# Optimization experiments

Measured on AMD Instinct MI355X. Metric: run time of the kernel, lower is better.

The kernel has to match this reference:

```python
import jax, jax.numpy as jnp
import numpy as np

B, S, D = 4, 2048, 1024
H, HD = 16, 64  # n_heads, head_dim (n_kv_heads == n_heads -> n_rep = 1)
WINDOW = 256
ROPE_THETA = 10000.0


def setup_inputs() -> dict:
    key = jax.random.key(0)
    ks = jax.random.split(key, 5)
    x = jax.random.normal(ks[0], (B, S, D), dtype=jnp.float32)
    scale = 0.02
    wq = jax.random.normal(ks[1], (D, D), dtype=jnp.float32) * scale
    wk = jax.random.normal(ks[2], (D, D), dtype=jnp.float32) * scale
    wv = jax.random.normal(ks[3], (D, D), dtype=jnp.float32) * scale
    wo = jax.random.normal(ks[4], (D, D), dtype=jnp.float32) * scale
    # RoPE frequencies: freqs_cis[t, i] = exp(1j * t / theta^(2i/HD)), i in [0, HD/2)
    inv_freq = 1.0 / (ROPE_THETA ** (jnp.arange(0, HD, 2, dtype=jnp.float32) / HD))
    t = jnp.arange(S, dtype=jnp.float32)
    ang = t[:, None] * inv_freq[None, :]  # [S, HD/2]
    return {"x": x, "freqs_cos": jnp.cos(ang), "freqs_sin": jnp.sin(ang),
            "wq": wq, "wk": wk, "wv": wv, "wo": wo}


def _apply_rope(xq, xk, cos, sin):
    # xq/xk: [B, S, H, HD]; cos/sin: [S, HD/2] broadcast as [1, S, 1, HD/2]
    def rot(v):
        vr = v.reshape(*v.shape[:-1], HD // 2, 2)
        v0, v1 = vr[..., 0], vr[..., 1]
        c = cos[None, :, None, :]
        s = sin[None, :, None, :]
        o0 = v0 * c - v1 * s
        o1 = v0 * s + v1 * c
        return jnp.stack([o0, o1], axis=-1).reshape(v.shape)
    return rot(xq), rot(xk)


def reference(x, freqs_cos, freqs_sin, wq, wk, wv, wo):
    b, s, _ = x.shape
    xq = (x @ wq.T).reshape(b, s, H, HD)
    xk = (x @ wk.T).reshape(b, s, H, HD)
    xv = (x @ wv.T).reshape(b, s, H, HD)
    xq, xk = _apply_rope(xq, xk, freqs_cos, freqs_sin)
    # [B, H, S, S] scores
    scores = jnp.einsum('bqhd,bkhd->bhqk', xq, xk) / jnp.sqrt(jnp.float32(HD))
    pos = jnp.arange(s)
    # masked (disallowed) when j > i (future) or i - j >= window
    bad = (pos[None, :] > pos[:, None]) | (pos[:, None] - pos[None, :] >= WINDOW)
    scores = jnp.where(bad[None, None], -jnp.inf, scores)
    attn = jax.nn.softmax(scores.astype(jnp.float32), axis=-1).astype(xq.dtype)
    out = jnp.einsum('bhqk,bkhd->bqhd', attn, xv).reshape(b, s, H * HD)
    return out @ wo.T
```

## Files before the change

### kernel.cpp

```cpp
#include <hip/hip_runtime.h>
#include <hip/hip_bf16.h>


typedef __bf16 bf16_t;
typedef __attribute__((ext_vector_type(8))) __bf16 bf16x8;
typedef __attribute__((ext_vector_type(4))) __bf16 bf16x4;
typedef __attribute__((ext_vector_type(4))) float f32x4;

#define MFMA16(a, b, c) __builtin_amdgcn_mfma_f32_16x16x32_bf16((a), (b), (c), 0, 0, 0)

__device__ __forceinline__ void async16(const void* g, void* l) {
    __builtin_amdgcn_global_load_lds(
        (const __attribute__((address_space(1))) unsigned int*)g,
        (__attribute__((address_space(3))) unsigned int*)l, 16, 0, 0);
}

#define BAR() do { asm volatile("" ::: "memory"); __builtin_amdgcn_s_barrier(); \
                   asm volatile("" ::: "memory"); } while (0)
#define VMC(N) asm volatile("s_waitcnt vmcnt(" #N ")" ::: "memory")

__global__ __launch_bounds__(256) void cvt_all(const float* __restrict__ x,
                                               const float* __restrict__ wq,
                                               const float* __restrict__ wk,
                                               const float* __restrict__ wv,
                                               const float* __restrict__ wo,
                                               bf16_t* __restrict__ xbf,
                                               bf16_t* __restrict__ wqkv,
                                               bf16_t* __restrict__ wobf) {
    const int blk = blockIdx.x;
    const float* s;
    bf16_t* d;
    int base;
    if (blk < 4096)      { s = x;  d = xbf;            base = blk; }
    else if (blk < 4608) { s = wq; d = wqkv;           base = blk - 4096; }
    else if (blk < 5120) { s = wk; d = wqkv + 1048576; base = blk - 4608; }
    else if (blk < 5632) { s = wv; d = wqkv + 2097152; base = blk - 5120; }
    else                 { s = wo; d = wobf;           base = blk - 5632; }
    const int i = (base * 256 + threadIdx.x) * 8;
    float4 a = *(const float4*)(s + i);
    float4 b = *(const float4*)(s + i + 4);
    bf16x8 o;
    o[0] = (bf16_t)a.x; o[1] = (bf16_t)a.y; o[2] = (bf16_t)a.z; o[3] = (bf16_t)a.w;
    o[4] = (bf16_t)b.x; o[5] = (bf16_t)b.y; o[6] = (bf16_t)b.z; o[7] = (bf16_t)b.w;
    *(bf16x8*)(d + i) = o;
}

__global__ __launch_bounds__(512, 1) __attribute__((amdgpu_waves_per_eu(2)))
void gemm192_qkv(const bf16_t* __restrict__ A, const bf16_t* __restrict__ Bw,
                 const float* __restrict__ fcos, const float* __restrict__ fsin,
                 bf16_t* __restrict__ Qo, bf16_t* __restrict__ Ko,
                 bf16_t* __restrict__ Vtmp, int M, int N, int K) {
    __shared__ __attribute__((aligned(16))) bf16_t As[32768];
    __shared__ __attribute__((aligned(16))) bf16_t Bs[24576];
    const int tid = threadIdx.x;
    const int l = tid & 63, w = tid >> 6;
    const int lr = l & 15, lg = l >> 4;
    const int wr = w >> 2, wc = w & 3;

    const int nwg = gridDim.x * gridDim.y;
    const int flat = blockIdx.y * gridDim.x + blockIdx.x;
    const int swz = (flat & 7) * (nwg >> 3) + (flat >> 3);
    const int bx = swz % gridDim.x, by = swz / gridDim.x;
    const long m0 = (long)by * 256, n0 = (long)bx * 192;
    const int NT = K >> 6;
    const int NI = NT >> 1;

    const int p  = w * 1024 + l * 16;
    const int pp = p ^ (((p >> 9) & 1) << 5);
    const int st = pp >> 10;
    const int rSt = (st >> 1) * 16 + ((pp >> 6) & 15);
    const int cSt = (st & 1) * 32 + ((pp >> 4) & 3) * 8;
    const bf16_t* aS = A  + (m0 + rSt) * K + cSt;
    const bf16_t* bS = Bw + (n0 + rSt) * K + cSt;
    const long uK = 64L * K;

    auto stageA = [&](int b, int u, int t) {
        async16(aS + (long)u * uK + (long)t * 64,
                (char*)As + b * 32768 + u * 8192 + w * 1024);
    };
    auto stageB = [&](int b, int u, int t) {
        async16(bS + (long)u * uK + (long)t * 64,
                (char*)Bs + b * 24576 + u * 8192 + w * 1024);
    };

    f32x4 acc[8][3] = {};
    bf16x8 afX[4], afY[4], bfX[3], bfY[3];
    const int swd = (lr & 8) << 2;

    auto loadAF = [&](int b, int mh, int ks, bf16x8 (&dst)[4]) {
#pragma unroll
        for (int mi = 0; mi < 4; ++mi) {
            const int off = (wr * 2 + mh) * 8192 + (mi * 2 + ks) * 1024 +
                            lr * 64 + lg * 16;
            dst[mi] = *(const bf16x8*)((const char*)As + b * 32768 + (off ^ swd));
        }
    };
    auto loadBF = [&](int b, int ks, bf16x8 (&dst)[3]) {
#pragma unroll
        for (int nj = 0; nj < 3; ++nj) {
            const int rg = wc * 48 + nj * 16 + lr;
            const int off = (rg >> 6) * 8192 + (((rg >> 4) & 3) * 2 + ks) * 1024 +
                            lr * 64 + lg * 16;
            dst[nj] = *(const bf16x8*)((const char*)Bs + b * 24576 + (off ^ swd));
        }
    };

#define QMM(MH, AF, BF) do {                                                   \
    __builtin_amdgcn_s_setprio(1);                                             \
    _Pragma("unroll")                                                          \
    for (int mi = 0; mi < 4; ++mi)                                             \
        _Pragma("unroll")                                                      \
        for (int nj = 0; nj < 3; ++nj)                                         \
            acc[(MH)*4+mi][nj] = MFMA16((AF)[mi], (BF)[nj], acc[(MH)*4+mi][nj]); \
    __builtin_amdgcn_s_setprio(0);                                             \
} while (0)

    stageA(0, 0, 0); stageA(0, 1, 0); stageA(0, 2, 0); stageA(0, 3, 0);
    stageB(0, 0, 0); stageB(0, 1, 0); stageB(0, 2, 0);
    stageB(1, 0, 1); stageB(1, 1, 1); stageB(1, 2, 1);
    VMC(3);
    BAR();

#pragma unroll 1
    for (int it = 0; it < NI - 1; ++it) {
        const int T = 2 * it;
        loadAF(0, 0, 0, afX); loadBF(0, 0, bfX);
        stageA(1, 0, T + 1); stageA(1, 1, T + 1);
        BAR(); QMM(0, afX, bfX); BAR();
        loadAF(0, 1, 0, afY);
        stageA(1, 2, T + 1); stageA(1, 3, T + 1);
        BAR(); QMM(1, afY, bfX); BAR();
        loadAF(0, 0, 1, afX); loadBF(0, 1, bfY);
        BAR(); QMM(0, afX, bfY); BAR();
        loadAF(0, 1, 1, afY);
        stageB(0, 0, T + 2);
        BAR(); QMM(1, afY, bfY); VMC(1); BAR();
        loadAF(1, 0, 0, afX); loadBF(1, 0, bfX);
        stageB(0, 1, T + 2); stageB(0, 2, T + 2);
        BAR(); QMM(0, afX, bfX); BAR();
        loadAF(1, 1, 0, afY);
        stageA(0, 0, T + 2); stageA(0, 1, T + 2);
        BAR(); QMM(1, afY, bfX); BAR();
        loadAF(1, 0, 1, afX); loadBF(1, 1, bfY);
        stageA(0, 2, T + 2); stageA(0, 3, T + 2);
        BAR(); QMM(0, afX, bfY); BAR();
        loadAF(1, 1, 1, afY);
        stageB(1, 0, T + 3); stageB(1, 1, T + 3); stageB(1, 2, T + 3);
        BAR(); QMM(1, afY, bfY); VMC(3); BAR();
    }

    {
        loadAF(0, 0, 0, afX); loadBF(0, 0, bfX);
        stageA(1, 0, NT - 1); stageA(1, 1, NT - 1);
        BAR(); QMM(0, afX, bfX); BAR();
        loadAF(0, 1, 0, afY);
        stageA(1, 2, NT - 1); stageA(1, 3, NT - 1);
        BAR(); QMM(1, afY, bfX); BAR();
        loadAF(0, 0, 1, afX); loadBF(0, 1, bfY);
        BAR(); QMM(0, afX, bfY); BAR();
        loadAF(0, 1, 1, afY);
        BAR(); QMM(1, afY, bfY);
        VMC(0); BAR();
        loadAF(1, 0, 0, afX); loadBF(1, 0, bfX);
        QMM(0, afX, bfX);
        loadAF(1, 1, 0, afY);
        QMM(1, afY, bfX);
        loadAF(1, 0, 1, afX); loadBF(1, 1, bfY);
        QMM(0, afX, bfY);
        loadAF(1, 1, 1, afY);
        QMM(1, afY, bfY);
    }
#undef QMM

#pragma unroll
    for (int nj = 0; nj < 3; ++nj) {
        const int cbase = (int)n0 + wc * 48 + nj * 16;
        const int cls = cbase >> 10;
        const int c = cbase + lr;
        if (cls == 2) {
            bf16_t* vp = Vtmp + (c - 2048);
#pragma unroll
            for (int ai = 0; ai < 8; ++ai)
#pragma unroll
                for (int j = 0; j < 4; ++j) {
                    const long t = m0 + wr * 128 + ai * 16 + lg * 4 + j;
                    vp[t * 1024] = (bf16_t)acc[ai][nj][j];
                }
        } else {
            const int d = c & 63;
            const int p2 = d >> 1;
            const int h = (c >> 6) & 15;
            const float sgn = (lr & 1) ? 1.f : -1.f;
            bf16_t* qk = (cls == 0) ? Qo : Ko;
#pragma unroll
            for (int ai = 0; ai < 8; ++ai)
#pragma unroll
                for (int j = 0; j < 4; ++j) {
                    const long t = m0 + wr * 128 + ai * 16 + lg * 4 + j;
                    const int s = (int)(t & 2047);
                    const int bb = (int)(t >> 11);
                    const float v = acc[ai][nj][j];
                    const float pv = __shfl_xor(v, 1);
                    const float cc = fcos[s * 32 + p2];
                    const float ss = fsin[s * 32 + p2];
                    const float o = v * cc + sgn * (pv * ss);
                    qk[((long)(bb * 16 + h) * 2048 + s) * 64 + d] = (bf16_t)o;
                }
        }
    }
}

__global__ __launch_bounds__(256) void vt_transpose(const bf16_t* __restrict__ V,
                                                    bf16_t* __restrict__ VT) {
    __shared__ __attribute__((aligned(16))) bf16_t vt[64][72];
    const int blk = blockIdx.x;
    const int st = blk & 31, bh = blk >> 5;
    const int h = bh & 15, b = bh >> 4;
    const int s0 = st << 6;
    const int tid = threadIdx.x;
    const int i = tid >> 2, dq = (tid & 3) << 4;
    const int s = s0 + i;

    const bf16_t* base = V + (long)(b * 2048 + s) * 1024 + h * 64 + dq;
    bf16x8 v0v = *(const bf16x8*)(base);
    bf16x8 v1v = *(const bf16x8*)(base + 8);

    *(bf16x8*)&vt[i][dq] = v0v;
    *(bf16x8*)&vt[i][dq + 8] = v1v;
    __syncthreads();
    const int d = tid >> 2, sb = (tid & 3) << 4;
    bf16x8 o0, o1;
#pragma unroll
    for (int j = 0; j < 8; ++j) {
        const int f = ((j & 3) << 1) | ((j >> 2) & 1);
        o0[j] = vt[sb + f][d];
        o1[j] = vt[sb + 8 + f][d];
    }
    const long va = ((long)bh * 64 + d) * 2048 + s0 + sb;
    *(bf16x8*)(VT + va) = o0;
    *(bf16x8*)(VT + va + 8) = o1;
}

template <typename OUT>
__global__ __launch_bounds__(512, 2) void gemm256(const bf16_t* __restrict__ A,
                                                  const bf16_t* __restrict__ Bw,
                                                  OUT* __restrict__ C,
                                                  int M, int N, int K) {
    __shared__ __attribute__((aligned(16))) bf16_t As[49152];
    __shared__ __attribute__((aligned(16))) bf16_t Bs[24576];
    const int tid = threadIdx.x;
    const int l = tid & 63, w = tid >> 6;
    const int lr = l & 15, lg = l >> 4;
    const int wr = w >> 1, wc = w & 1;

    const int nwg = gridDim.x * gridDim.y;
    const int flat = blockIdx.y * gridDim.x + blockIdx.x;
    const int swz = (flat & 7) * (nwg >> 3) + (flat >> 3);
    const int bx = swz % gridDim.x, by = swz / gridDim.x;
    const long m0 = (long)by * 256, n0 = (long)bx * 128;
    const int NT = K >> 6;

    int rS[2], cS[2];
#pragma unroll
    for (int i = 0; i < 2; ++i) {
        const int p  = i * 8192 + w * 1024 + l * 16;
        const int pp = p ^ (((p >> 9) & 1) << 5);
        const int st = pp >> 10;
        rS[i] = (st >> 1) * 16 + ((pp >> 6) & 15);
        cS[i] = (st & 1) * 32 + ((pp >> 4) & 3) * 8;
    }
    const bf16_t* aSrc0 = A  + (m0 + rS[0]) * K + cS[0];
    const bf16_t* aSrc1 = A  + (m0 + rS[1]) * K + cS[1];
    const bf16_t* bSrc0 = Bw + (n0 + rS[0]) * K + cS[0];
    const bf16_t* bSrc1 = Bw + (n0 + rS[1]) * K + cS[1];
    const long hK = 128L * K;

    auto stageA = [&](int b, int h, int t) {
        char* d = (char*)As + b * 32768 + h * 16384 + w * 1024;
        const long o = (long)h * hK + (long)t * 64;
        async16(aSrc0 + o, d);
        async16(aSrc1 + o, d + 8192);
    };
    auto stageB = [&](int b, int t) {
        char* d = (char*)Bs + b * 16384 + w * 1024;
        const long o = (long)t * 64;
        async16(bSrc0 + o, d);
        async16(bSrc1 + o, d + 8192);
    };

    f32x4 acc[4][4] = {};
    bf16x8 af[4][2], blo[2][2], bhi[2][2];
    const int swd = (lr & 8) << 2;

    auto loadA = [&](int b) {
#pragma unroll
        for (int mi = 0; mi < 4; ++mi)
#pragma unroll
            for (int ks = 0; ks < 2; ++ks) {
                const int ra = (wr & 1) * 64 + mi * 16 + lr;
                const int off = ((ra >> 4) * 2 + ks) * 1024 + (ra & 15) * 64 + lg * 16;
                af[mi][ks] = *(const bf16x8*)((const char*)As + b * 32768 +
                                              (wr >> 1) * 16384 + (off ^ swd));
            }
    };
    auto loadB = [&](int b, int nh, bf16x8 (&dst)[2][2]) {
#pragma unroll
        for (int nj = 0; nj < 2; ++nj)
#pragma unroll
            for (int ks = 0; ks < 2; ++ks) {
                const int rb = wc * 64 + (nh * 2 + nj) * 16 + lr;
                const int off = ((rb >> 4) * 2 + ks) * 1024 + (rb & 15) * 64 + lg * 16;
                dst[nj][ks] = *(const bf16x8*)((const char*)Bs + b * 16384 +
                                               (off ^ swd));
            }
    };

#define QMM(NH, BF) do {                                                       \
    __builtin_amdgcn_s_setprio(1);                                             \
    _Pragma("unroll")                                                          \
    for (int mi = 0; mi < 4; ++mi) {                                           \
        acc[mi][(NH)*2]   = MFMA16(af[mi][0], (BF)[0][0], acc[mi][(NH)*2]);    \
        acc[mi][(NH)*2]   = MFMA16(af[mi][1], (BF)[0][1], acc[mi][(NH)*2]);    \
        acc[mi][(NH)*2+1] = MFMA16(af[mi][0], (BF)[1][0], acc[mi][(NH)*2+1]);  \
        acc[mi][(NH)*2+1] = MFMA16(af[mi][1], (BF)[1][1], acc[mi][(NH)*2+1]);  \
    }                                                                          \
    __builtin_amdgcn_s_setprio(0);                                             \
} while (0)

    stageA(0, 0, 0); stageA(0, 1, 0); stageB(0, 0);
    stageA(1, 0, 1); stageA(1, 1, 1); stageB(1, 1);
    VMC(6);
    BAR();

    int bc = 0;
#pragma unroll 1
    for (int t = 0; t < NT - 2; ++t) {
        const int bn = (bc + 2 >= 3) ? bc - 1 : bc + 2;
        loadA(bc); loadB(bc, 0, blo); stageA(bn, 0, t + 2); stageA(bn, 1, t + 2);
        BAR(); QMM(0, blo); BAR();
        loadB(bc, 1, bhi); stageB(bn, t + 2);
        BAR(); QMM(1, bhi);
        if (t < NT - 3) { VMC(6); } else { VMC(0); }
        BAR();
        bc = (bc + 1 >= 3) ? 0 : bc + 1;
    }
    {
        loadA(bc); loadB(bc, 0, blo);
        QMM(0, blo);
        loadB(bc, 1, bhi);
        QMM(1, bhi);
        const int b2 = (bc + 1 >= 3) ? 0 : bc + 1;
        loadA(b2); loadB(b2, 0, blo);
        QMM(0, blo);
        loadB(b2, 1, bhi);
        QMM(1, bhi);
    }
#undef QMM

#pragma unroll
    for (int mi = 0; mi < 4; ++mi)
#pragma unroll
        for (int ni = 0; ni < 4; ++ni)
#pragma unroll
            for (int j = 0; j < 4; ++j) {
                long r = m0 + wr * 64 + mi * 16 + lg * 4 + j;
                long c = n0 + wc * 64 + ni * 16 + lr;
                C[r * N + c] = (OUT)acc[mi][ni][j];
            }
}

__global__ __launch_bounds__(256, 2) void attn_win4(const bf16_t* __restrict__ Q,
                                                    const bf16_t* __restrict__ Kb,
                                                    const bf16_t* __restrict__ VT,
                                                    bf16_t* __restrict__ Ao) {
    __shared__ __attribute__((aligned(16))) bf16_t kld[5 * 4096];
    __shared__ __attribute__((aligned(16))) bf16_t vld[5 * 4096];
    const int raw = blockIdx.x;
    const int mswz = ((raw & 7) << 8) | (raw >> 3);
    const int qt = mswz & 31, bh = mswz >> 5;
    const int h = bh & 15, b = bh >> 4;
    const int l = threadIdx.x & 63, w = threadIdx.x >> 6;
    const int lr = l & 15, lg = l >> 4;
    const int q0 = qt * 64 + w * 16;
    const int q = q0 + lr;
    const int tb = qt - 4;

    const bf16_t* Qp = Q + (long)bh * 2048 * 64;
    const bf16_t* Kp = Kb + (long)bh * 2048 * 64;
    const bf16_t* Vp = VT + (long)bh * 64 * 2048;

#pragma unroll
    for (int u = 0; u < 5; ++u) {
        const int kt = tb + u;
        const int kt64 = (kt < 0 ? 0 : kt) * 64;
#pragma unroll
        for (int part = 0; part < 2; ++part) {
            const int seg = w * 2 + part;
            const int r = seg * 8 + (l >> 3);
            const int sc = (l & 7) ^ ((r >> 1) & 7);
            async16(Kp + (long)(kt64 + r) * 64 + sc * 8,
                    (char*)kld + u * 8192 + seg * 1024);
            async16(Vp + (long)r * 2048 + kt64 + sc * 8,
                    (char*)vld + u * 8192 + seg * 1024);
        }
    }

    const bf16x8 qb0 = *(const bf16x8*)&Qp[q * 64 + lg * 8];
    const bf16x8 qb1 = *(const bf16x8*)&Qp[q * 64 + 32 + lg * 8];

    __syncthreads();

    float mrun = -1000.f, lsum = 0.f;
    f32x4 o0 = {0.f, 0.f, 0.f, 0.f}, o1 = {0.f, 0.f, 0.f, 0.f};
    f32x4 o2 = {0.f, 0.f, 0.f, 0.f}, o3 = {0.f, 0.f, 0.f, 0.f};
    const int swv = (lr >> 1) & 7;

    const char* kbase;
    const char* vbase;
    int k0s;

#define QKCORE(HH, MM)                                                           \
        const int row_ = (HH) * 32 + 2 * lr + (MM);                              \
        const int sw_ = (row_ >> 1) & 7;                                         \
        bf16x8 k0_ = *(const bf16x8*)(kbase + row_ * 128 + ((lg ^ sw_) << 4));   \
        bf16x8 k1_ = *(const bf16x8*)(kbase + row_ * 128 + (((4 + lg) ^ sw_) << 4)); \
        f32x4 s_ = {0.f, 0.f, 0.f, 0.f};                                         \
        s_ = MFMA16(k0_, qb0, s_);                                               \
        s_ = MFMA16(k1_, qb1, s_);

#define QKF_F(DST, HH, MM)                                                       \
    f32x4 DST; { QKCORE(HH, MM)                                                  \
        const int kb_ = k0s + (HH) * 32 + (MM) + lg * 8;                         \
        DST[0] = ((kb_ >= 0) & ((unsigned)(q - kb_) < 256u))         ? s_[0] * 0.125f : -1e30f; \
        DST[1] = ((kb_ + 2 >= 0) & ((unsigned)(q - kb_ - 2) < 256u)) ? s_[1] * 0.125f : -1e30f; \
        DST[2] = ((kb_ + 4 >= 0) & ((unsigned)(q - kb_ - 4) < 256u)) ? s_[2] * 0.125f : -1e30f; \
        DST[3] = ((kb_ + 6 >= 0) & ((unsigned)(q - kb_ - 6) < 256u)) ? s_[3] * 0.125f : -1e30f; \
    }

#define QKF_U(DST, HH, MM)                                                       \
    f32x4 DST; { QKCORE(HH, MM)                                                  \
        const int d_ = q - (k0s + (HH) * 32 + (MM) + lg * 8);                    \
        DST[0] = (d_ < 256)     ? s_[0] * 0.125f : -1e30f;                       \
        DST[1] = (d_ - 2 < 256) ? s_[1] * 0.125f : -1e30f;                       \
        DST[2] = (d_ - 4 < 256) ? s_[2] * 0.125f : -1e30f;                       \
        DST[3] = (d_ - 6 < 256) ? s_[3] * 0.125f : -1e30f;                       \
    }

#define QKF_L(DST, HH, MM)                                                       \
    f32x4 DST; { QKCORE(HH, MM)                                                  \
        const int d_ = q - (k0s + (HH) * 32 + (MM) + lg * 8);                    \
        DST[0] = (d_ >= 0)     ? s_[0] * 0.125f : -1e30f;                        \
        DST[1] = (d_ - 2 >= 0) ? s_[1] * 0.125f : -1e30f;                        \
        DST[2] = (d_ - 4 >= 0) ? s_[2] * 0.125f : -1e30f;                        \
        DST[3] = (d_ - 6 >= 0) ? s_[3] * 0.125f : -1e30f;                        \
    }

#define QKF_N(DST, HH, MM)                                                       \
    f32x4 DST; { QKCORE(HH, MM)                                                  \
        DST[0] = s_[0] * 0.125f; DST[1] = s_[1] * 0.125f;                        \
        DST[2] = s_[2] * 0.125f; DST[3] = s_[3] * 0.125f;                        \
    }

#define EXV(S_) {                                                                \
        S_[0] = __expf(S_[0] - mnew); S_[1] = __expf(S_[1] - mnew);              \
        S_[2] = __expf(S_[2] - mnew); S_[3] = __expf(S_[3] - mnew);              \
        rs += (S_[0] + S_[1]) + (S_[2] + S_[3]); }

#define PVF(NT, HH, PB) {                                                        \
        bf16x8 va_ = *(const bf16x8*)(vbase + ((NT) * 16 + lr) * 128 +           \
                                      ((((HH) * 4 + lg) ^ swv) << 4));           \
        o##NT = MFMA16(va_, PB, o##NT); }

#define TILEBODY(QKM) {                                                          \
        QKM(sA, 0, 0) QKM(sB, 0, 1) QKM(sC, 1, 0) QKM(sD, 1, 1)                  \
        float tm = fmaxf(fmaxf(fmaxf(sA[0], sA[1]), fmaxf(sA[2], sA[3])),        \
                         fmaxf(fmaxf(sB[0], sB[1]), fmaxf(sB[2], sB[3])));       \
        tm = fmaxf(tm, fmaxf(fmaxf(fmaxf(sC[0], sC[1]), fmaxf(sC[2], sC[3])),    \
                             fmaxf(fmaxf(sD[0], sD[1]), fmaxf(sD[2], sD[3]))));  \
        tm = fmaxf(tm, __shfl_xor(tm, 16));                                      \
        tm = fmaxf(tm, __shfl_xor(tm, 32));                                      \
        const float mnew = fmaxf(mrun, tm);                                      \
        const float alpha = __expf(mrun - mnew);                                 \
        mrun = mnew;                                                             \
        float rs = 0.f;                                                          \
        EXV(sA) EXV(sB) EXV(sC) EXV(sD)                                          \
        rs += __shfl_xor(rs, 16);                                                \
        rs += __shfl_xor(rs, 32);                                                \
        lsum = lsum * alpha + rs;                                                \
        o0[0] *= alpha; o0[1] *= alpha; o0[2] *= alpha; o0[3] *= alpha;          \
        o1[0] *= alpha; o1[1] *= alpha; o1[2] *= alpha; o1[3] *= alpha;          \
        o2[0] *= alpha; o2[1] *= alpha; o2[2] *= alpha; o2[3] *= alpha;          \
        o3[0] *= alpha; o3[1] *= alpha; o3[2] *= alpha; o3[3] *= alpha;          \
        bf16x8 pb0, pb1;                                                         \
        pb0[0] = (bf16_t)sA[0]; pb0[1] = (bf16_t)sA[1]; pb0[2] = (bf16_t)sA[2]; pb0[3] = (bf16_t)sA[3]; \
        pb0[4] = (bf16_t)sB[0]; pb0[5] = (bf16_t)sB[1]; pb0[6] = (bf16_t)sB[2]; pb0[7] = (bf16_t)sB[3]; \
        pb1[0] = (bf16_t)sC[0]; pb1[1] = (bf16_t)sC[1]; pb1[2] = (bf16_t)sC[2]; pb1[3] = (bf16_t)sC[3]; \
        pb1[4] = (bf16_t)sD[0]; pb1[5] = (bf16_t)sD[1]; pb1[6] = (bf16_t)sD[2]; pb1[7] = (bf16_t)sD[3]; \
        PVF(0, 0, pb0) PVF(1, 0, pb0) PVF(2, 0, pb0) PVF(3, 0, pb0)              \
        PVF(0, 1, pb1) PVF(1, 1, pb1) PVF(2, 1, pb1) PVF(3, 1, pb1)              \
    }

#define SETT(U) kbase = (const char*)kld + (U) * 8192;                           \
                vbase = (const char*)vld + (U) * 8192;                           \
                k0s = (tb + (U)) * 64;

    if (qt >= 4) {
        SETT(0) TILEBODY(QKF_U)
        SETT(1) TILEBODY(QKF_N)
        SETT(2) TILEBODY(QKF_N)
        SETT(3) TILEBODY(QKF_N)
        SETT(4) TILEBODY(QKF_L)
    } else {
#pragma unroll
        for (int u = 0; u < 5; ++u) {
            SETT(u) TILEBODY(QKF_F)
        }
    }
#undef SETT
#undef TILEBODY
#undef QKF_F
#undef QKF_U
#undef QKF_L
#undef QKF_N
#undef QKCORE
#undef EXV
#undef PVF

    const float rinv = 1.0f / lsum;
    bf16_t* aor = Ao + ((long)(b * 2048) + q) * 1024 + h * 64;
#define EPI(NT, OA_) {                                                           \
        bf16x4 ov_;                                                             \
        ov_[0] = (bf16_t)(OA_[0] * rinv); ov_[1] = (bf16_t)(OA_[1] * rinv);      \
        ov_[2] = (bf16_t)(OA_[2] * rinv); ov_[3] = (bf16_t)(OA_[3] * rinv);      \
        *(bf16x4*)(aor + (NT) * 16 + lg * 4) = ov_; }
    EPI(0, o0) EPI(1, o1) EPI(2, o2) EPI(3, o3)
#undef EPI
}

extern "C" void kernel_launch(void* const* d_in, const int* in_sizes, int n_in,
                              void* d_out, int out_size, void* d_ws, size_t ws_size,
                              hipStream_t stream) {
    (void)in_sizes; (void)n_in; (void)out_size; (void)ws_size;
    const float* x    = (const float*)d_in[0];
    const float* fcos = (const float*)d_in[1];
    const float* fsin = (const float*)d_in[2];
    const float* wq   = (const float*)d_in[3];
    const float* wk   = (const float*)d_in[4];
    const float* wv   = (const float*)d_in[5];
    const float* wo   = (const float*)d_in[6];
    float* out = (float*)d_out;

    char* ws = (char*)d_ws;
    bf16_t* xbf  = (bf16_t*)(ws);
    bf16_t* wqkv = (bf16_t*)(ws + 16777216);
    bf16_t* wobf = (bf16_t*)(ws + 23068672);
    bf16_t* vtmp = (bf16_t*)(ws + 25165824);
    bf16_t* qbuf = (bf16_t*)(ws + 41943040);
    bf16_t* kbuf = (bf16_t*)(ws + 75497472);
    bf16_t* vtb  = (bf16_t*)(ws + 92274688);
    bf16_t* aob  = xbf;

    cvt_all<<<6144, 256, 0, stream>>>(x, wq, wk, wv, wo, xbf, wqkv, wobf);

    gemm192_qkv<<<dim3(16, 32), 512, 0, stream>>>(xbf, wqkv, fcos, fsin,
                                                  qbuf, kbuf, vtmp,
                                                  8192, 3072, 1024);
    vt_transpose<<<2048, 256, 0, stream>>>(vtmp, vtb);
    attn_win4<<<2048, 256, 0, stream>>>(qbuf, kbuf, vtb, aob);
    gemm256<float><<<dim3(8, 32), 512, 0, stream>>>(aob, wobf, out, 8192, 1024, 1024);
}
```

Baseline: 130.1 us.

## Fuse V transpose into QKV GEMM epilogue and transpose RoPE tables

The QKV GEMM epilogue now stages V tiles through reused LDS scratch and writes them directly in the transposed per-head layout that attention expects. This removes the separate vt_transpose kernel and its extra round trip of V through global memory. RoPE cos/sin tables are also transposed once inside the conversion kernel, so the Q/K epilogue can load them as float4 along the sequence axis. The cost is a more complex epilogue that depends on LDS reuse after the main loop having no hazards.

After: 126.9 us. 2.5% less time.

```diff
diff --git a/kernel.cpp b/kernel.cpp
--- a/kernel.cpp
+++ b/kernel.cpp
@@ -18,16 +18,29 @@
 #define BAR() do { asm volatile("" ::: "memory"); __builtin_amdgcn_s_barrier(); \
                    asm volatile("" ::: "memory"); } while (0)
 #define VMC(N) asm volatile("s_waitcnt vmcnt(" #N ")" ::: "memory")
+#define LGKM0() asm volatile("s_waitcnt lgkmcnt(0)" ::: "memory")
 
 __global__ __launch_bounds__(256) void cvt_all(const float* __restrict__ x,
                                                const float* __restrict__ wq,
                                                const float* __restrict__ wk,
                                                const float* __restrict__ wv,
                                                const float* __restrict__ wo,
+                                               const float* __restrict__ fcos,
+                                               const float* __restrict__ fsin,
                                                bf16_t* __restrict__ xbf,
                                                bf16_t* __restrict__ wqkv,
-                                               bf16_t* __restrict__ wobf) {
+                                               bf16_t* __restrict__ wobf,
+                                               float* __restrict__ fcosT,
+                                               float* __restrict__ fsinT) {
     const int blk = blockIdx.x;
+    if (blk >= 6144) {
+        const int p = blk - 6144;
+        for (int s = threadIdx.x; s < 2048; s += 256) {
+            fcosT[p * 2048 + s] = fcos[s * 32 + p];
+            fsinT[p * 2048 + s] = fsin[s * 32 + p];
+        }
+        return;
+    }
     const float* s;
     bf16_t* d;
     int base;
@@ -47,9 +60,9 @@
 
 __global__ __launch_bounds__(512, 1) __attribute__((amdgpu_waves_per_eu(2)))
 void gemm192_qkv(const bf16_t* __restrict__ A, const bf16_t* __restrict__ Bw,
-                 const float* __restrict__ fcos, const float* __restrict__ fsin,
+                 const float* __restrict__ fcosT, const float* __restrict__ fsinT,
                  bf16_t* __restrict__ Qo, bf16_t* __restrict__ Ko,
-                 bf16_t* __restrict__ Vtmp, int M, int N, int K) {
+                 bf16_t* __restrict__ VT, int M, int N, int K) {
     __shared__ __attribute__((aligned(16))) bf16_t As[32768];
     __shared__ __attribute__((aligned(16))) bf16_t Bs[24576];
     const int tid = threadIdx.x;
@@ -172,73 +185,71 @@
     }
 #undef QMM
 
+    bf16_t* scr = (w < 6) ? (bf16_t*)((char*)As + w * 4608)
+                          : (bf16_t*)((char*)Bs + (w - 6) * 4608);
+    asm volatile("" ::: "memory");
+
 #pragma unroll
     for (int nj = 0; nj < 3; ++nj) {
         const int cbase = (int)n0 + wc * 48 + nj * 16;
         const int cls = cbase >> 10;
-        const int c = cbase + lr;
         if (cls == 2) {
-            bf16_t* vp = Vtmp + (c - 2048);
 #pragma unroll
             for (int ai = 0; ai < 8; ++ai)
 #pragma unroll
-                for (int j = 0; j < 4; ++j) {
-                    const long t = m0 + wr * 128 + ai * 16 + lg * 4 + j;
-                    vp[t * 1024] = (bf16_t)acc[ai][nj][j];
+                for (int j = 0; j < 4; ++j)
+                    scr[(ai * 16 + lg * 4 + j) * 18 + lr] = (bf16_t)acc[ai][nj][j];
+            LGKM0();
+            asm volatile("" ::: "memory");
+            const int ch = l & 15;
+            const int g0 = l >> 4;
+            const int d16 = cbase - 2048 + ch;
+            const int hh = d16 >> 6, dd = d16 & 63;
+            const long T0 = m0 + wr * 128;
+            const int bb = (int)(T0 >> 11);
+            const int s0 = (int)(T0 & 2047);
+            bf16_t* vrow = VT + ((long)((bb * 16 + hh) * 64 + dd) * 2048) + s0;
+#pragma unroll
+            for (int qq = 0; qq < 4; ++qq) {
+                const int grp = g0 + qq * 4;
+                bf16x8 o;
+#pragma unroll
+                for (int j = 0; j < 8; ++j) {
+                    const int f = ((j & 3) << 1) | (j >> 2);
+                    o[j] = scr[(grp * 8 + f) * 18 + ch];
                 }
+                *(bf16x8*)(vrow + grp * 8) = o;
+            }
+            LGKM0();
+            asm volatile("" ::: "memory");
         } else {
-            const int d = c & 63;
-            const int p2 = d >> 1;
-            const int h = (c >> 6) & 15;
+            const int c = cbase + lr;
+            const int dd = c & 63;
+            const int p2 = dd >> 1;
+            const int hh = (c >> 6) & 15;
             const float sgn = (lr & 1) ? 1.f : -1.f;
             bf16_t* qk = (cls == 0) ? Qo : Ko;
-#pragma unroll
-            for (int ai = 0; ai < 8; ++ai)
-#pragma unroll
-                for (int j = 0; j < 4; ++j) {
-                    const long t = m0 + wr * 128 + ai * 16 + lg * 4 + j;
-                    const int s = (int)(t & 2047);
-                    const int bb = (int)(t >> 11);
-                    const float v = acc[ai][nj][j];
-                    const float pv = __shfl_xor(v, 1);
-                    const float cc = fcos[s * 32 + p2];
-                    const float ss = fsin[s * 32 + p2];
-                    const float o = v * cc + sgn * (pv * ss);
-                    qk[((long)(bb * 16 + h) * 2048 + s) * 64 + d] = (bf16_t)o;
-                }
+            const float* cT = fcosT + p2 * 2048;
+            const float* sT = fsinT + p2 * 2048;
+#pragma unroll
+            for (int ai = 0; ai < 8; ++ai) {
+                const long t0 = m0 + wr * 128 + ai * 16 + lg * 4;
+                const int s0 = (int)(t0 & 2047);
+                const int bb = (int)(t0 >> 11);
+                const float4 cc = *(const float4*)(cT + s0);
+                const float4 ss = *(const float4*)(sT + s0);
+                bf16_t* row = qk + ((long)(bb * 16 + hh) * 2048 + s0) * 64 + dd;
+                const float v0 = acc[ai][nj][0], pv0 = __shfl_xor(acc[ai][nj][0], 1);
+                const float v1 = acc[ai][nj][1], pv1 = __shfl_xor(acc[ai][nj][1], 1);
+                const float v2 = acc[ai][nj][2], pv2 = __shfl_xor(acc[ai][nj][2], 1);
+                const float v3 = acc[ai][nj][3], pv3 = __shfl_xor(acc[ai][nj][3], 1);
+                row[0]       = (bf16_t)(v0 * cc.x + sgn * (pv0 * ss.x));
+                row[64]      = (bf16_t)(v1 * cc.y + sgn * (pv1 * ss.y));
+                row[128]     = (bf16_t)(v2 * cc.z + sgn * (pv2 * ss.z));
+                row[192]     = (bf16_t)(v3 * cc.w + sgn * (pv3 * ss.w));
+            }
         }
     }
-}
-
-__global__ __launch_bounds__(256) void vt_transpose(const bf16_t* __restrict__ V,
-                                                    bf16_t* __restrict__ VT) {
-    __shared__ __attribute__((aligned(16))) bf16_t vt[64][72];
-    const int blk = blockIdx.x;
-    const int st = blk & 31, bh = blk >> 5;
-    const int h = bh & 15, b = bh >> 4;
-    const int s0 = st << 6;
-    const int tid = threadIdx.x;
-    const int i = tid >> 2, dq = (tid & 3) << 4;
-    const int s = s0 + i;
-
-    const bf16_t* base = V + (long)(b * 2048 + s) * 1024 + h * 64 + dq;
-    bf16x8 v0v = *(const bf16x8*)(base);
-    bf16x8 v1v = *(const bf16x8*)(base + 8);
-
-    *(bf16x8*)&vt[i][dq] = v0v;
-    *(bf16x8*)&vt[i][dq + 8] = v1v;
-    __syncthreads();
-    const int d = tid >> 2, sb = (tid & 3) << 4;
-    bf16x8 o0, o1;
-#pragma unroll
-    for (int j = 0; j < 8; ++j) {
-        const int f = ((j & 3) << 1) | ((j >> 2) & 1);
-        o0[j] = vt[sb + f][d];
-        o1[j] = vt[sb + 8 + f][d];
-    }
-    const long va = ((long)bh * 64 + d) * 2048 + s0 + sb;
-    *(bf16x8*)(VT + va) = o0;
-    *(bf16x8*)(VT + va + 8) = o1;
 }
 
 template <typename OUT>
@@ -551,21 +562,22 @@
     float* out = (float*)d_out;
 
     char* ws = (char*)d_ws;
-    bf16_t* xbf  = (bf16_t*)(ws);
-    bf16_t* wqkv = (bf16_t*)(ws + 16777216);
-    bf16_t* wobf = (bf16_t*)(ws + 23068672);
-    bf16_t* vtmp = (bf16_t*)(ws + 25165824);
-    bf16_t* qbuf = (bf16_t*)(ws + 41943040);
-    bf16_t* kbuf = (bf16_t*)(ws + 75497472);
-    bf16_t* vtb  = (bf16_t*)(ws + 92274688);
-    bf16_t* aob  = xbf;
-
-    cvt_all<<<6144, 256, 0, stream>>>(x, wq, wk, wv, wo, xbf, wqkv, wobf);
-
-    gemm192_qkv<<<dim3(16, 32), 512, 0, stream>>>(xbf, wqkv, fcos, fsin,
-                                                  qbuf, kbuf, vtmp,
+    bf16_t* xbf   = (bf16_t*)(ws);
+    bf16_t* wqkv  = (bf16_t*)(ws + 16777216);
+    bf16_t* wobf  = (bf16_t*)(ws + 23068672);
+    float*  fcosT = (float*)(ws + 25165824);
+    float*  fsinT = (float*)(ws + 25427968);
+    bf16_t* qbuf  = (bf16_t*)(ws + 41943040);
+    bf16_t* kbuf  = (bf16_t*)(ws + 75497472);
+    bf16_t* vtb   = (bf16_t*)(ws + 92274688);
+    bf16_t* aob   = xbf;
+
+    cvt_all<<<6176, 256, 0, stream>>>(x, wq, wk, wv, wo, fcos, fsin,
+                                      xbf, wqkv, wobf, fcosT, fsinT);
+
+    gemm192_qkv<<<dim3(16, 32), 512, 0, stream>>>(xbf, wqkv, fcosT, fsinT,
+                                                  qbuf, kbuf, vtb,
                                                   8192, 3072, 1024);
-    vt_transpose<<<2048, 256, 0, stream>>>(vtmp, vtb);
     attn_win4<<<2048, 256, 0, stream>>>(qbuf, kbuf, vtb, aob);
     gemm256<float><<<dim3(8, 32), 512, 0, stream>>>(aob, wobf, out, 8192, 1024, 1024);
 }
```
